# Optimization experiments

Measured on AMD Instinct MI355X. Metric: run time of the kernel, lower is better.

## Reference

```python
import jax, jax.numpy as jnp
import numpy as np

M = 10000      # spans with antecedents
KMAX = 30      # max antecedents per span
N = 12000      # total candidate spans (rows of g_i)
GDIM = 512     # span embedding dim
DDIM, GEDIM, SDIM = 20, 20, 20  # distance / genre / speaker embed dims
HID = 150      # Score hidden dim
GIJ = 3 * GDIM + DDIM + GEDIM + SDIM  # 1596
NDIST, NGENRE, NSPK = 10, 7, 3


def setup_inputs() -> dict:
    rng = np.random.default_rng(0)
    lengths = rng.integers(1, KMAX + 1, size=M)           # antecedents per span
    P = int(lengths.sum())
    seg_ids = np.repeat(np.arange(1, M + 1), lengths).astype(np.int32)  # segment 0 is the leading empty split
    pos_in_seg = np.concatenate([np.arange(l) for l in lengths]).astype(np.int32)
    seg_lengths = np.concatenate([[0], lengths]).astype(np.int32)        # [S], S = M+1
    mention_ids = rng.integers(0, N, size=P).astype(np.int32)
    antecedent_ids = rng.integers(0, N, size=P).astype(np.int32)
    dist_idx = rng.integers(0, NDIST, size=P).astype(np.int32)
    genre_idx = rng.integers(0, NGENRE, size=P).astype(np.int32)
    speaker_idx = rng.integers(0, NSPK, size=P).astype(np.int32)

    ks = jax.random.split(jax.random.key(0), 12)
    sc = lambda d: 1.0 / np.sqrt(d)
    return {
        'g_i': jax.random.normal(ks[0], (N, GDIM), jnp.float32),
        'mention_scores': jax.random.normal(ks[1], (N, 1), jnp.float32),
        'dist_emb': jax.random.normal(ks[2], (NDIST, DDIM), jnp.float32),
        'genre_emb': jax.random.normal(ks[3], (NGENRE, GEDIM), jnp.float32),
        'speaker_emb': jax.random.normal(ks[4], (NSPK, SDIM), jnp.float32),
        'W1': jax.random.normal(ks[5], (GIJ, HID), jnp.float32) * sc(GIJ),
        'b1': jnp.zeros((HID,), jnp.float32),
        'W2': jax.random.normal(ks[6], (HID, HID), jnp.float32) * sc(HID),
        'b2': jnp.zeros((HID,), jnp.float32),
        'W3': jax.random.normal(ks[7], (HID, 1), jnp.float32) * sc(HID),
        'b3': jnp.zeros((1,), jnp.float32),
        'mention_ids': jnp.asarray(mention_ids),
        'antecedent_ids': jnp.asarray(antecedent_ids),
        'dist_idx': jnp.asarray(dist_idx),
        'genre_idx': jnp.asarray(genre_idx),
        'speaker_idx': jnp.asarray(speaker_idx),
        'seg_ids': jnp.asarray(seg_ids),
        'pos_in_seg': jnp.asarray(pos_in_seg),
        'seg_lengths': jnp.asarray(seg_lengths),
    }


def reference(g_i, mention_scores, dist_emb, genre_emb, speaker_emb,
              W1, b1, W2, b2, W3, b3,
              mention_ids, antecedent_ids, dist_idx, genre_idx, speaker_idx,
              seg_ids, pos_in_seg, seg_lengths):
    # phi = cat(distance, genre, speaker) side features, [P, 60]
    phi = jnp.concatenate([dist_emb[dist_idx], genre_emb[genre_idx], speaker_emb[speaker_idx]], axis=1)
    i_g = g_i[mention_ids]      # [P, GDIM] irregular gather
    j_g = g_i[antecedent_ids]   # [P, GDIM]
    pairs = jnp.concatenate([i_g, j_g, i_g * j_g, phi], axis=1)  # [P, GIJ]
    # 3-layer MLP scorer (dropout is identity at inference)
    h = jax.nn.relu(pairs @ W1 + b1)
    h = jax.nn.relu(h @ W2 + b2)
    s_ij = (h @ W3 + b3)[:, 0]  # [P]
    coref = mention_scores[mention_ids, 0] + mention_scores[antecedent_ids, 0] + s_ij  # [P]
    # variable-length segment softmax with epsilon=0 appended, padded with 1000
    S = seg_lengths.shape[0]
    dense = jnp.full((S, KMAX + 1), -jnp.inf, jnp.float32)
    dense = dense.at[seg_ids, pos_in_seg].set(coref)
    dense = dense.at[jnp.arange(S), seg_lengths].set(0.0)  # epsilon slot
    probs = jax.nn.softmax(dense, axis=1)  # -inf slots -> 0
    col = jnp.arange(KMAX + 1)
    probs = jnp.where(col[None, :] > seg_lengths[:, None], 1000.0, probs)  # pad value 1000
    return probs  # [S, KMAX+1]
```

## Files before the change

### kernel.cpp

```cpp
#include <hip/hip_runtime.h>
#include <stdint.h>

#define GDIM   512
#define HID    150
#define HIDP   160
#define NROWS  12000
#define KP1    31
#define BMP    128
#define BMF    256

typedef __attribute__((ext_vector_type(4))) float f32x4;
typedef __attribute__((ext_vector_type(2))) float f32x2;
typedef long i64;

__device__ __forceinline__ unsigned short f2bf(float x){
    unsigned int u = __float_as_uint(x);
    return (unsigned short)((u + 0x7fffu + ((u >> 16) & 1u)) >> 16);
}
__device__ __forceinline__ float bf2f(unsigned short u){
    return __uint_as_float(((unsigned int)u) << 16);
}
__device__ __forceinline__ i64 u2l(uint2 v){ return __builtin_bit_cast(i64, v); }
__device__ __forceinline__ f32x4 mfma8(i64 a, i64 b, f32x4 c){
    return __builtin_amdgcn_mfma_f32_16x16x32_fp8_fp8(a, b, c, 0, 0, 0);
}
__device__ __forceinline__ uint2 f8mulpk(uint2 m, uint2 a){
    f32x2 m0 = __builtin_amdgcn_cvt_pk_f32_fp8(m.x, false);
    f32x2 m1 = __builtin_amdgcn_cvt_pk_f32_fp8(m.x, true);
    f32x2 m2 = __builtin_amdgcn_cvt_pk_f32_fp8(m.y, false);
    f32x2 m3 = __builtin_amdgcn_cvt_pk_f32_fp8(m.y, true);
    f32x2 a0 = __builtin_amdgcn_cvt_pk_f32_fp8(a.x, false);
    f32x2 a1 = __builtin_amdgcn_cvt_pk_f32_fp8(a.x, true);
    f32x2 a2 = __builtin_amdgcn_cvt_pk_f32_fp8(a.y, false);
    f32x2 a3 = __builtin_amdgcn_cvt_pk_f32_fp8(a.y, true);
    unsigned int r0 = 0, r1 = 0;
    r0 = __builtin_amdgcn_cvt_pk_fp8_f32(m0[0]*a0[0], m0[1]*a0[1], r0, false);
    r0 = __builtin_amdgcn_cvt_pk_fp8_f32(m1[0]*a1[0], m1[1]*a1[1], r0, true);
    r1 = __builtin_amdgcn_cvt_pk_fp8_f32(m2[0]*a2[0], m2[1]*a2[1], r1, false);
    r1 = __builtin_amdgcn_cvt_pk_fp8_f32(m3[0]*a3[0], m3[1]*a3[1], r1, true);
    return (uint2){r0, r1};
}
__device__ __forceinline__ void glds16(const void* g, void* l){
    __builtin_amdgcn_global_load_lds(
        (const __attribute__((address_space(1))) unsigned int*)g,
        (__attribute__((address_space(3))) unsigned int*)l, 16, 0, 0);
}

__global__ void k_prep0(const float* __restrict__ g, unsigned char* __restrict__ g8,
                        int* __restrict__ hist, int4* __restrict__ recs,
                        const float* __restrict__ W1, unsigned char* __restrict__ W18,
                        const float* __restrict__ W2, unsigned char* __restrict__ W28, int P){
    int i = blockIdx.x * blockDim.x + threadIdx.x;
    if (i < NROWS) hist[i] = 0;
    if (i < BMF) recs[P + i] = (int4){0, 0, (int)0x80000000, 0};
    if (i < 30720){
        int s = i / 10240, r = i % 10240;
        int n = r >> 6, gi = r & 63;
        int gdst = gi ^ (n & 7);
        int k0 = s * 512 + gi * 8;
        float x[8];
        #pragma unroll
        for (int e = 0; e < 8; e++) x[e] = (n < HID) ? W1[(size_t)(k0 + e) * HID + n] : 0.f;
        unsigned int d0 = 0, d1 = 0;
        d0 = __builtin_amdgcn_cvt_pk_fp8_f32(x[0], x[1], d0, false);
        d0 = __builtin_amdgcn_cvt_pk_fp8_f32(x[2], x[3], d0, true);
        d1 = __builtin_amdgcn_cvt_pk_fp8_f32(x[4], x[5], d1, false);
        d1 = __builtin_amdgcn_cvt_pk_fp8_f32(x[6], x[7], d1, true);
        *reinterpret_cast<uint2*>(W18 + (size_t)s * 81920 + n * 512 + gdst * 8) = (uint2){d0, d1};
    }
    if (i < 6912){
        int n2 = i / 42, kd = (i % 42) * 4;
        float y[4];
        #pragma unroll
        for (int e = 0; e < 4; e++){
            int k = kd + e;
            y[e] = (n2 < HID && k < HID) ? W2[(size_t)k * HID + n2] : 0.f;
        }
        unsigned int d = 0;
        d = __builtin_amdgcn_cvt_pk_fp8_f32(y[0], y[1], d, false);
        d = __builtin_amdgcn_cvt_pk_fp8_f32(y[2], y[3], d, true);
        reinterpret_cast<unsigned int*>(W28)[i] = d;
    }
    if (i >= NROWS * 32) return;
    int lh = i & 3, kt = (i >> 2) & 7, row = i >> 5;
    const float* src = g + (size_t)row * 512 + kt * 64 + lh * 8;
    float4 x0 = *reinterpret_cast<const float4*>(src);
    float4 x1 = *reinterpret_cast<const float4*>(src + 4);
    float4 x2 = *reinterpret_cast<const float4*>(src + 32);
    float4 x3 = *reinterpret_cast<const float4*>(src + 36);
    uint4 o; unsigned int d;
    d = 0; d = __builtin_amdgcn_cvt_pk_fp8_f32(x0.x, x0.y, d, false);
    d = __builtin_amdgcn_cvt_pk_fp8_f32(x0.z, x0.w, d, true);  o.x = d;
    d = 0; d = __builtin_amdgcn_cvt_pk_fp8_f32(x1.x, x1.y, d, false);
    d = __builtin_amdgcn_cvt_pk_fp8_f32(x1.z, x1.w, d, true);  o.y = d;
    d = 0; d = __builtin_amdgcn_cvt_pk_fp8_f32(x2.x, x2.y, d, false);
    d = __builtin_amdgcn_cvt_pk_fp8_f32(x2.z, x2.w, d, true);  o.z = d;
    d = 0; d = __builtin_amdgcn_cvt_pk_fp8_f32(x3.x, x3.y, d, false);
    d = __builtin_amdgcn_cvt_pk_fp8_f32(x3.z, x3.w, d, true);  o.w = d;
    *reinterpret_cast<uint4*>(g8 + (size_t)row * 512 + kt * 64 + lh * 16) = o;
}

__global__ void k_wprep(const float* __restrict__ de, const float* __restrict__ ge,
                        const float* __restrict__ se, const float* __restrict__ W1,
                        const float* __restrict__ b1,
                        const float* __restrict__ W3, const float* __restrict__ b2,
                        unsigned short* __restrict__ PhiW,
                        float* __restrict__ w3p, float* __restrict__ b2p){
    int c = blockIdx.x, tid = threadIdx.x;
    if (c < 210 && tid < HIDP){
        int si = c % 3, gi2 = (c / 3) % 7, di = c / 21;
        float acc = 0.f;
        if (tid < HID){
            acc = b1[tid];
            #pragma unroll
            for (int dd = 0; dd < 20; dd++) acc += de[di*20 + dd] * W1[(size_t)(1536 + dd) * HID + tid];
            #pragma unroll
            for (int dd = 0; dd < 20; dd++) acc += ge[gi2*20 + dd] * W1[(size_t)(1556 + dd) * HID + tid];
            #pragma unroll
            for (int dd = 0; dd < 20; dd++) acc += se[si*20 + dd] * W1[(size_t)(1576 + dd) * HID + tid];
        }
        PhiW[c * HIDP + tid] = f2bf(acc);
    }
    if (c == 210 && tid < HIDP){
        w3p[tid] = (tid < HID) ? W3[tid] : 0.f;
        b2p[tid] = (tid < HID) ? b2[tid] : 0.f;
    }
}

__global__ void k_hist(const int* __restrict__ mid, int* __restrict__ hist, int P){
    int p = blockIdx.x * blockDim.x + threadIdx.x;
    if (p < P) atomicAdd(&hist[mid[p]], 1);
}
__global__ void k_scan(const int* __restrict__ hist, int* __restrict__ offsw, int nb){
    __shared__ int part[1024];
    int t = threadIdx.x;
    int chunk = (nb + 1023) / 1024;
    int lo = t * chunk, hi = lo + chunk; if (hi > nb) hi = nb;
    int s = 0;
    for (int b = lo; b < hi; b++) s += hist[b];
    part[t] = s;
    __syncthreads();
    for (int d = 1; d < 1024; d <<= 1){
        int v = (t >= d) ? part[t - d] : 0;
        __syncthreads();
        part[t] += v;
        __syncthreads();
    }
    int run = part[t] - s;
    for (int b = lo; b < hi; b++){ offsw[b] = run; run += hist[b]; }
}
__global__ void k_scatter(const int* __restrict__ mident, const int* __restrict__ antid,
                          const int* __restrict__ di, const int* __restrict__ gi, const int* __restrict__ si,
                          const int* __restrict__ seg, const int* __restrict__ pos, const float* __restrict__ ms,
                          int* __restrict__ offsw, int4* __restrict__ recs, int P){
    int p = blockIdx.x * blockDim.x + threadIdx.x;
    if (p >= P) return;
    int m = mident[p], a = antid[p];
    int idx = atomicAdd(&offsw[m], 1);
    int combo = (di[p] * 7 + gi[p]) * 3 + si[p];
    int meta = (combo << 19) | (seg[p] << 5) | pos[p];
    int4 r; r.x = m; r.y = a; r.z = meta; r.w = __float_as_int(ms[m] + ms[a]);
    recs[idx] = r;
}

__global__ __launch_bounds__(256) void k_proj(const unsigned char* __restrict__ g8,
                                              const unsigned char* __restrict__ W18,
                                              unsigned char* __restrict__ out){
    __shared__ __align__(16) char smem[81920];
    const unsigned char* Wt = W18 + (size_t)blockIdx.y * 81920;
    unsigned char* outh = out + (size_t)blockIdx.y * NROWS * HIDP;
    int tid = threadIdx.x, lane = tid & 63, w = tid >> 6;
    int l15 = lane & 15, lh = lane >> 4;
    int swz8 = (l15 & 7) << 3;
    int row0 = blockIdx.x * BMP;

    int r0 = row0 + 32*w + l15;       int r0c = (r0 < NROWS) ? r0 : NROWS - 1;
    int r1 = r0 + 16;                 int r1c = (r1 < NROWS) ? r1 : NROWS - 1;
    const unsigned char* gp0 = g8 + (size_t)r0c * GDIM + lh * 16;
    const unsigned char* gp1 = g8 + (size_t)r1c * GDIM + lh * 16;

    #pragma unroll
    for (int i = 0; i < 20; i++){
        int c = w * 20 + i;
        glds16(Wt + c * 1024 + lane * 16, smem + c * 1024);
    }

    f32x4 acc1[10][2];
    #pragma unroll
    for (int t = 0; t < 10; t++){ acc1[t][0] = (f32x4){0,0,0,0}; acc1[t][1] = (f32x4){0,0,0,0}; }

    asm volatile("s_waitcnt vmcnt(0)" ::: "memory");
    __builtin_amdgcn_s_barrier();

    uint4 R0 = *reinterpret_cast<const uint4*>(gp0);
    uint4 R1 = *reinterpret_cast<const uint4*>(gp1);
    #pragma unroll
    for (int kt = 0; kt < 8; kt++){
        uint4 N0, N1;
        if (kt < 7){
            N0 = *reinterpret_cast<const uint4*>(gp0 + (kt+1)*64);
            N1 = *reinterpret_cast<const uint4*>(gp1 + (kt+1)*64);
        }
        i64 a00 = u2l((uint2){R0.x, R0.y}), a01 = u2l((uint2){R0.z, R0.w});
        i64 a10 = u2l((uint2){R1.x, R1.y}), a11 = u2l((uint2){R1.z, R1.w});
        #pragma unroll
        for (int t = 0; t < 10; t++){
            int rowb = (t*16 + l15) * 512;
            i64 b0 = *reinterpret_cast<const i64*>(&smem[rowb + ((kt*64 +  0 + lh*8) ^ swz8)]);
            i64 b1 = *reinterpret_cast<const i64*>(&smem[rowb + ((kt*64 + 32 + lh*8) ^ swz8)]);
            acc1[t][0] = mfma8(b0, a00, acc1[t][0]);
            acc1[t][1] = mfma8(b0, a10, acc1[t][1]);
            acc1[t][0] = mfma8(b1, a01, acc1[t][0]);
            acc1[t][1] = mfma8(b1, a11, acc1[t][1]);
        }
        R0 = N0; R1 = N1;
    }

    #pragma unroll
    for (int rf = 0; rf < 2; rf++){
        int row = row0 + 32*w + 16*rf + l15;
        if (row < NROWS){
            #pragma unroll
            for (int t = 0; t < 10; t++){
                f32x4 a = acc1[t][rf];
                unsigned int dw = 0;
                dw = __builtin_amdgcn_cvt_pk_fp8_f32(a[0], a[1], dw, false);
                dw = __builtin_amdgcn_cvt_pk_fp8_f32(a[2], a[3], dw, true);
                *reinterpret_cast<unsigned int*>(outh + (size_t)row * HIDP + 16*t + 4*lh) = dw;
            }
        }
    }
}

__global__ __launch_bounds__(512, 2) void k_fused(
    const unsigned char* __restrict__ g8,
    const unsigned char* __restrict__ W1c8, const unsigned char* __restrict__ W28,
    const unsigned short* __restrict__ PhiW, const unsigned char* __restrict__ Am,
    const unsigned char* __restrict__ Aa,
    const float* __restrict__ w3p, const float* __restrict__ b2p, const float* __restrict__ b3,
    const int4* __restrict__ recs,
    float* __restrict__ dense)
{
    __shared__ __align__(16) char smem[81920];
    int tid = threadIdx.x, lane = tid & 63, w = tid >> 6;
    int l15 = lane & 15, lh = lane >> 4;
    int swz8 = (l15 & 7) << 3;

    int nwg = gridDim.x, orig = blockIdx.x, bid = orig;
    if (nwg >= 8){
        int q = nwg >> 3, r = nwg & 7;
        int xcd = orig & 7, lid = orig >> 3;
        bid = (xcd < r ? xcd * (q + 1) : r * (q + 1) + (xcd - r) * q) + lid;
    }
    int p0 = bid * BMF;

    int4 rec0 = recs[p0 + 32*w + l15];
    int4 rec1 = recs[p0 + 32*w + 16 + l15];

    const unsigned char* gm0 = g8 + (size_t)rec0.x * GDIM + lh * 16;
    const unsigned char* ga0 = g8 + (size_t)rec0.y * GDIM + lh * 16;
    const unsigned char* gm1 = g8 + (size_t)rec1.x * GDIM + lh * 16;
    const unsigned char* ga1 = g8 + (size_t)rec1.y * GDIM + lh * 16;

    #pragma unroll
    for (int i = 0; i < 10; i++){
        int c = w * 10 + i;
        glds16(W1c8 + c * 1024 + lane * 16, smem + c * 1024);
    }

    f32x4 acc1[10][2];
    #pragma unroll
    for (int t = 0; t < 10; t++){ acc1[t][0] = (f32x4){0,0,0,0}; acc1[t][1] = (f32x4){0,0,0,0}; }

    asm volatile("s_waitcnt vmcnt(0)" ::: "memory");
    __builtin_amdgcn_s_barrier();

    uint4 Rm0 = *reinterpret_cast<const uint4*>(gm0);
    uint4 Ra0 = *reinterpret_cast<const uint4*>(ga0);
    uint4 Rm1 = *reinterpret_cast<const uint4*>(gm1);
    uint4 Ra1 = *reinterpret_cast<const uint4*>(ga1);
    #pragma unroll
    for (int kt = 0; kt < 8; kt++){
        uint4 Nm0, Na0, Nm1, Na1;
        if (kt < 7){
            Nm0 = *reinterpret_cast<const uint4*>(gm0 + (kt+1)*64);
            Na0 = *reinterpret_cast<const uint4*>(ga0 + (kt+1)*64);
            Nm1 = *reinterpret_cast<const uint4*>(gm1 + (kt+1)*64);
            Na1 = *reinterpret_cast<const uint4*>(ga1 + (kt+1)*64);
        }
        uint2 p00 = f8mulpk((uint2){Rm0.x, Rm0.y}, (uint2){Ra0.x, Ra0.y});
        uint2 p01 = f8mulpk((uint2){Rm0.z, Rm0.w}, (uint2){Ra0.z, Ra0.w});
        uint2 p10 = f8mulpk((uint2){Rm1.x, Rm1.y}, (uint2){Ra1.x, Ra1.y});
        uint2 p11 = f8mulpk((uint2){Rm1.z, Rm1.w}, (uint2){Ra1.z, Ra1.w});
        i64 lp00 = u2l(p00), lp01 = u2l(p01), lp10 = u2l(p10), lp11 = u2l(p11);
        #pragma unroll
        for (int t = 0; t < 10; t++){
            int rowb = (t*16 + l15) * 512;
            i64 b0 = *reinterpret_cast<const i64*>(&smem[rowb + ((kt*64 +  0 + lh*8) ^ swz8)]);
            i64 b1 = *reinterpret_cast<const i64*>(&smem[rowb + ((kt*64 + 32 + lh*8) ^ swz8)]);
            acc1[t][0] = mfma8(b0, lp00, acc1[t][0]);
            acc1[t][1] = mfma8(b0, lp10, acc1[t][1]);
            acc1[t][0] = mfma8(b1, lp01, acc1[t][0]);
            acc1[t][1] = mfma8(b1, lp11, acc1[t][1]);
        }
        Rm0 = Nm0; Ra0 = Na0; Rm1 = Nm1; Ra1 = Na1;
    }

    asm volatile("s_waitcnt lgkmcnt(0)" ::: "memory");
    __builtin_amdgcn_s_barrier();

    #pragma unroll
    for (int i = 0; i < 4; i++){
        int c = w * 4 + i;
        if (c < 27) glds16(W28 + c * 1024 + lane * 16, smem + 43008 + c * 1024);
    }

    #pragma unroll
    for (int rf = 0; rf < 2; rf++){
        int4 rc = rf ? rec1 : rec0;
        int pr = 32*w + 16*rf + l15;
        const unsigned char* amp = Am + (size_t)rc.x * HIDP;
        const unsigned char* aap = Aa + (size_t)rc.y * HIDP;
        int combo = (rc.z >> 19) & 0xFF;
        const unsigned short* php = PhiW + (size_t)combo * HIDP;
        char* h1row = smem + pr * 168;
        #pragma unroll
        for (int t = 0; t < 10; t++){
            int h0 = 16*t + 4*lh;
            unsigned int amd = *reinterpret_cast<const unsigned int*>(amp + h0);
            unsigned int aad = *reinterpret_cast<const unsigned int*>(aap + h0);
            ushort4 ph4 = *reinterpret_cast<const ushort4*>(php + h0);
            f32x2 amL = __builtin_amdgcn_cvt_pk_f32_fp8(amd, false);
            f32x2 amH = __builtin_amdgcn_cvt_pk_f32_fp8(amd, true);
            f32x2 aaL = __builtin_amdgcn_cvt_pk_f32_fp8(aad, false);
            f32x2 aaH = __builtin_amdgcn_cvt_pk_f32_fp8(aad, true);
            f32x4 a = acc1[t][rf];
            float v0 = fmaxf(a[0] + amL[0] + aaL[0] + bf2f(ph4.x), 0.f);
            float v1 = fmaxf(a[1] + amL[1] + aaL[1] + bf2f(ph4.y), 0.f);
            float v2 = fmaxf(a[2] + amH[0] + aaH[0] + bf2f(ph4.z), 0.f);
            float v3 = fmaxf(a[3] + amH[1] + aaH[1] + bf2f(ph4.w), 0.f);
            unsigned int dw = 0;
            dw = __builtin_amdgcn_cvt_pk_fp8_f32(v0, v1, dw, false);
            dw = __builtin_amdgcn_cvt_pk_fp8_f32(v2, v3, dw, true);
            *reinterpret_cast<unsigned int*>(h1row + h0) = dw;
        }
    }

    asm volatile("s_waitcnt vmcnt(0) lgkmcnt(0)" ::: "memory");
    __builtin_amdgcn_s_barrier();

    f32x4 acc2[10][2];
    #pragma unroll
    for (int t = 0; t < 10; t++){ acc2[t][0] = (f32x4){0,0,0,0}; acc2[t][1] = (f32x4){0,0,0,0}; }
    const char* w2b = smem + 43008;
    #pragma unroll
    for (int k2 = 0; k2 < 5; k2++){
        i64 h0f = *reinterpret_cast<const i64*>(smem + (32*w + l15)      * 168 + k2*32 + lh*8);
        i64 h1f = *reinterpret_cast<const i64*>(smem + (32*w + 16 + l15) * 168 + k2*32 + lh*8);
        #pragma unroll
        for (int t = 0; t < 10; t++){
            i64 wf = *reinterpret_cast<const i64*>(w2b + (16*t + l15) * 168 + k2*32 + lh*8);
            acc2[t][0] = mfma8(wf, h0f, acc2[t][0]);
            acc2[t][1] = mfma8(wf, h1f, acc2[t][1]);
        }
    }

    float b3v = b3[0];
    #pragma unroll
    for (int rf = 0; rf < 2; rf++){
        int4 rc = rf ? rec1 : rec0;
        float s = 0.f;
        #pragma unroll
        for (int t = 0; t < 10; t++){
            f32x4 w3v = *reinterpret_cast<const f32x4*>(w3p + 16*t + 4*lh);
            f32x4 b2v = *reinterpret_cast<const f32x4*>(b2p + 16*t + 4*lh);
            f32x4 a = acc2[t][rf];
            s += fmaxf(a[0] + b2v[0], 0.f) * w3v[0];
            s += fmaxf(a[1] + b2v[1], 0.f) * w3v[1];
            s += fmaxf(a[2] + b2v[2], 0.f) * w3v[2];
            s += fmaxf(a[3] + b2v[3], 0.f) * w3v[3];
        }
        s += __shfl_xor(s, 16);
        s += __shfl_xor(s, 32);
        if (!(rc.z & 0x80000000) && lh == 0){
            float val = s + b3v + __int_as_float(rc.w);
            dense[(size_t)((rc.z >> 5) & 0x3FFF) * KP1 + (rc.z & 31)] = val;
        }
    }
}

__global__ void k_softmax(const float* __restrict__ dense, const int* __restrict__ seg_lengths,
                          float* __restrict__ out, int S){
    int wid = threadIdx.x >> 6, lane = threadIdx.x & 63;
    int s = blockIdx.x * 4 + wid;
    if (s >= S) return;
    int len = seg_lengths[s];
    float ninf = -__builtin_inff();
    float val = ninf;
    if (lane < KP1) val = (lane < len) ? dense[(size_t)s * KP1 + lane] : ((lane == len) ? 0.f : ninf);
    float m = val;
    #pragma unroll
    for (int msk = 1; msk < 64; msk <<= 1) m = fmaxf(m, __shfl_xor(m, msk));
    float e = expf(val - m);
    float sum = e;
    #pragma unroll
    for (int msk = 1; msk < 64; msk <<= 1) sum += __shfl_xor(sum, msk);
    if (lane < KP1) out[(size_t)s * KP1 + lane] = (lane > len) ? 1000.f : (e / sum);
}

extern "C" void kernel_launch(void* const* d_in, const int* in_sizes, int n_in,
                              void* d_out, int out_size, void* d_ws, size_t ws_size,
                              hipStream_t stream){
    const float* g_i        = (const float*)d_in[0];
    const float* ms         = (const float*)d_in[1];
    const float* dist_emb   = (const float*)d_in[2];
    const float* genre_emb  = (const float*)d_in[3];
    const float* spk_emb    = (const float*)d_in[4];
    const float* W1         = (const float*)d_in[5];
    const float* b1         = (const float*)d_in[6];
    const float* W2         = (const float*)d_in[7];
    const float* b2         = (const float*)d_in[8];
    const float* W3         = (const float*)d_in[9];
    const float* b3         = (const float*)d_in[10];
    const int* mention_ids  = (const int*)d_in[11];
    const int* antecedent_ids = (const int*)d_in[12];
    const int* dist_idx     = (const int*)d_in[13];
    const int* genre_idx    = (const int*)d_in[14];
    const int* spk_idx      = (const int*)d_in[15];
    const int* seg_ids      = (const int*)d_in[16];
    const int* pos_in_seg   = (const int*)d_in[17];
    const int* seg_lengths  = (const int*)d_in[18];
    int P = in_sizes[11];
    int S = in_sizes[18];

    char* ws = (char*)d_ws;
    unsigned char* W18   = (unsigned char*)(ws + 0);
    unsigned char* W28   = (unsigned char*)(ws + 245760);
    unsigned short* PhiW = (unsigned short*)(ws + 273408);
    float* w3pad         = (float*)(ws + 340608);
    float* b2pad         = (float*)(ws + 341248);
    unsigned char* g8    = (unsigned char*)(ws + 341888);
    unsigned char* Am8   = (unsigned char*)(ws + 6485888);
    unsigned char* Aa8   = (unsigned char*)(ws + 8405888);
    int* hist            = (int*)(ws + 10325888);
    int* offsw           = (int*)(ws + 10373888);
    int4* recs           = (int4*)(ws + 10421888);
    float* dense         = (float*)(ws + 13000192);

    k_prep0<<<1500, 256, 0, stream>>>(g_i, g8, hist, recs, W1, W18, W2, W28, P);
    k_wprep<<<211, 256, 0, stream>>>(dist_emb, genre_emb, spk_emb, W1, b1, W3, b2,
                                     PhiW, w3pad, b2pad);
    k_hist<<<(P + 255)/256, 256, 0, stream>>>(mention_ids, hist, P);
    k_scan<<<1, 1024, 0, stream>>>(hist, offsw, NROWS);
    k_scatter<<<(P + 255)/256, 256, 0, stream>>>(mention_ids, antecedent_ids, dist_idx, genre_idx,
        spk_idx, seg_ids, pos_in_seg, ms, offsw, recs, P);

    k_proj<<<dim3((NROWS + BMP - 1)/BMP, 2), 256, 0, stream>>>(g8, W18, Am8);

    k_fused<<<(P + BMF - 1)/BMF, 512, 0, stream>>>(g8, W18 + 2*81920, W28, PhiW,
        Am8, Aa8, w3pad, b2pad, b3, recs, dense);

    k_softmax<<<(S + 3)/4, 256, 0, stream>>>(dense, seg_lengths, (float*)d_out, S);
}
```

Baseline: 129.5 us.

## Halve fused tile and LDS, stream W1 in two K-halves, merge prep kernels

```diff
diff --git a/kernel.cpp b/kernel.cpp
--- a/kernel.cpp
+++ b/kernel.cpp
@@ -7,7 +7,7 @@
 #define NROWS  12000
 #define KP1    31
 #define BMP    128
-#define BMF    256
+#define BMF    128
 
 typedef __attribute__((ext_vector_type(4))) float f32x4;
 typedef __attribute__((ext_vector_type(2))) float f32x2;
@@ -49,14 +49,20 @@
 __global__ void k_prep0(const float* __restrict__ g, unsigned char* __restrict__ g8,
                         int* __restrict__ hist, int4* __restrict__ recs,
                         const float* __restrict__ W1, unsigned char* __restrict__ W18,
-                        const float* __restrict__ W2, unsigned char* __restrict__ W28, int P){
+                        const float* __restrict__ W2, unsigned char* __restrict__ W28,
+                        const float* __restrict__ de, const float* __restrict__ ge,
+                        const float* __restrict__ se, const float* __restrict__ b1,
+                        const float* __restrict__ W3, const float* __restrict__ b2,
+                        unsigned short* __restrict__ PhiW,
+                        float* __restrict__ w3p, float* __restrict__ b2p, int P){
     int i = blockIdx.x * blockDim.x + threadIdx.x;
     if (i < NROWS) hist[i] = 0;
     if (i < BMF) recs[P + i] = (int4){0, 0, (int)0x80000000, 0};
     if (i < 30720){
         int s = i / 10240, r = i % 10240;
         int n = r >> 6, gi = r & 63;
-        int gdst = gi ^ (n & 7);
+        int hf = gi >> 5, gih = gi & 31;
+        int gdst = gih ^ (n & 7);
         int k0 = s * 512 + gi * 8;
         float x[8];
         #pragma unroll
@@ -66,7 +72,7 @@
         d0 = __builtin_amdgcn_cvt_pk_fp8_f32(x[2], x[3], d0, true);
         d1 = __builtin_amdgcn_cvt_pk_fp8_f32(x[4], x[5], d1, false);
         d1 = __builtin_amdgcn_cvt_pk_fp8_f32(x[6], x[7], d1, true);
-        *reinterpret_cast<uint2*>(W18 + (size_t)s * 81920 + n * 512 + gdst * 8) = (uint2){d0, d1};
+        *reinterpret_cast<uint2*>(W18 + (size_t)s * 81920 + hf * 40960 + n * 256 + gdst * 8) = (uint2){d0, d1};
     }
     if (i < 6912){
         int n2 = i / 42, kd = (i % 42) * 4;
@@ -81,49 +87,42 @@
         d = __builtin_amdgcn_cvt_pk_fp8_f32(y[2], y[3], d, true);
         reinterpret_cast<unsigned int*>(W28)[i] = d;
     }
-    if (i >= NROWS * 32) return;
-    int lh = i & 3, kt = (i >> 2) & 7, row = i >> 5;
-    const float* src = g + (size_t)row * 512 + kt * 64 + lh * 8;
-    float4 x0 = *reinterpret_cast<const float4*>(src);
-    float4 x1 = *reinterpret_cast<const float4*>(src + 4);
-    float4 x2 = *reinterpret_cast<const float4*>(src + 32);
-    float4 x3 = *reinterpret_cast<const float4*>(src + 36);
-    uint4 o; unsigned int d;
-    d = 0; d = __builtin_amdgcn_cvt_pk_fp8_f32(x0.x, x0.y, d, false);
-    d = __builtin_amdgcn_cvt_pk_fp8_f32(x0.z, x0.w, d, true);  o.x = d;
-    d = 0; d = __builtin_amdgcn_cvt_pk_fp8_f32(x1.x, x1.y, d, false);
-    d = __builtin_amdgcn_cvt_pk_fp8_f32(x1.z, x1.w, d, true);  o.y = d;
-    d = 0; d = __builtin_amdgcn_cvt_pk_fp8_f32(x2.x, x2.y, d, false);
-    d = __builtin_amdgcn_cvt_pk_fp8_f32(x2.z, x2.w, d, true);  o.z = d;
-    d = 0; d = __builtin_amdgcn_cvt_pk_fp8_f32(x3.x, x3.y, d, false);
-    d = __builtin_amdgcn_cvt_pk_fp8_f32(x3.z, x3.w, d, true);  o.w = d;
-    *reinterpret_cast<uint4*>(g8 + (size_t)row * 512 + kt * 64 + lh * 16) = o;
-}
-
-__global__ void k_wprep(const float* __restrict__ de, const float* __restrict__ ge,
-                        const float* __restrict__ se, const float* __restrict__ W1,
-                        const float* __restrict__ b1,
-                        const float* __restrict__ W3, const float* __restrict__ b2,
-                        unsigned short* __restrict__ PhiW,
-                        float* __restrict__ w3p, float* __restrict__ b2p){
-    int c = blockIdx.x, tid = threadIdx.x;
-    if (c < 210 && tid < HIDP){
+    if (i < NROWS * 32){
+        int lh = i & 3, kt = (i >> 2) & 7, row = i >> 5;
+        const float* src = g + (size_t)row * 512 + kt * 64 + lh * 8;
+        float4 x0 = *reinterpret_cast<const float4*>(src);
+        float4 x1 = *reinterpret_cast<const float4*>(src + 4);
+        float4 x2 = *reinterpret_cast<const float4*>(src + 32);
+        float4 x3 = *reinterpret_cast<const float4*>(src + 36);
+        uint4 o; unsigned int d;
+        d = 0; d = __builtin_amdgcn_cvt_pk_fp8_f32(x0.x, x0.y, d, false);
+        d = __builtin_amdgcn_cvt_pk_fp8_f32(x0.z, x0.w, d, true);  o.x = d;
+        d = 0; d = __builtin_amdgcn_cvt_pk_fp8_f32(x1.x, x1.y, d, false);
+        d = __builtin_amdgcn_cvt_pk_fp8_f32(x1.z, x1.w, d, true);  o.y = d;
+        d = 0; d = __builtin_amdgcn_cvt_pk_fp8_f32(x2.x, x2.y, d, false);
+        d = __builtin_amdgcn_cvt_pk_fp8_f32(x2.z, x2.w, d, true);  o.z = d;
+        d = 0; d = __builtin_amdgcn_cvt_pk_fp8_f32(x3.x, x3.y, d, false);
+        d = __builtin_amdgcn_cvt_pk_fp8_f32(x3.z, x3.w, d, true);  o.w = d;
+        *reinterpret_cast<uint4*>(g8 + (size_t)row * 512 + kt * 64 + lh * 16) = o;
+    } else if (i < NROWS * 32 + 33600){
+        int j = i - NROWS * 32;
+        int c = j / HIDP, h = j - c * HIDP;
         int si = c % 3, gi2 = (c / 3) % 7, di = c / 21;
         float acc = 0.f;
-        if (tid < HID){
-            acc = b1[tid];
-            #pragma unroll
-            for (int dd = 0; dd < 20; dd++) acc += de[di*20 + dd] * W1[(size_t)(1536 + dd) * HID + tid];
-            #pragma unroll
-            for (int dd = 0; dd < 20; dd++) acc += ge[gi2*20 + dd] * W1[(size_t)(1556 + dd) * HID + tid];
-            #pragma unroll
-            for (int dd = 0; dd < 20; dd++) acc += se[si*20 + dd] * W1[(size_t)(1576 + dd) * HID + tid];
-        }
-        PhiW[c * HIDP + tid] = f2bf(acc);
-    }
-    if (c == 210 && tid < HIDP){
-        w3p[tid] = (tid < HID) ? W3[tid] : 0.f;
-        b2p[tid] = (tid < HID) ? b2[tid] : 0.f;
+        if (h < HID){
+            acc = b1[h];
+            #pragma unroll
+            for (int dd = 0; dd < 20; dd++) acc += de[di*20 + dd] * W1[(size_t)(1536 + dd) * HID + h];
+            #pragma unroll
+            for (int dd = 0; dd < 20; dd++) acc += ge[gi2*20 + dd] * W1[(size_t)(1556 + dd) * HID + h];
+            #pragma unroll
+            for (int dd = 0; dd < 20; dd++) acc += se[si*20 + dd] * W1[(size_t)(1576 + dd) * HID + h];
+        }
+        PhiW[c * HIDP + h] = f2bf(acc);
+    } else if (i < NROWS * 32 + 33600 + HIDP){
+        int h = i - NROWS * 32 - 33600;
+        w3p[h] = (h < HID) ? W3[h] : 0.f;
+        b2p[h] = (h < HID) ? b2[h] : 0.f;
     }
 }
 
@@ -166,7 +165,7 @@
 __global__ __launch_bounds__(256) void k_proj(const unsigned char* __restrict__ g8,
                                               const unsigned char* __restrict__ W18,
                                               unsigned char* __restrict__ out){
-    __shared__ __align__(16) char smem[81920];
+    __shared__ __align__(16) char smem[40960];
     const unsigned char* Wt = W18 + (size_t)blockIdx.y * 81920;
     unsigned char* outh = out + (size_t)blockIdx.y * NROWS * HIDP;
     int tid = threadIdx.x, lane = tid & 63, w = tid >> 6;
@@ -179,41 +178,47 @@
     const unsigned char* gp0 = g8 + (size_t)r0c * GDIM + lh * 16;
     const unsigned char* gp1 = g8 + (size_t)r1c * GDIM + lh * 16;
 
-    #pragma unroll
-    for (int i = 0; i < 20; i++){
-        int c = w * 20 + i;
-        glds16(Wt + c * 1024 + lane * 16, smem + c * 1024);
-    }
-
     f32x4 acc1[10][2];
     #pragma unroll
     for (int t = 0; t < 10; t++){ acc1[t][0] = (f32x4){0,0,0,0}; acc1[t][1] = (f32x4){0,0,0,0}; }
 
-    asm volatile("s_waitcnt vmcnt(0)" ::: "memory");
-    __builtin_amdgcn_s_barrier();
-
-    uint4 R0 = *reinterpret_cast<const uint4*>(gp0);
-    uint4 R1 = *reinterpret_cast<const uint4*>(gp1);
-    #pragma unroll
-    for (int kt = 0; kt < 8; kt++){
-        uint4 N0, N1;
-        if (kt < 7){
-            N0 = *reinterpret_cast<const uint4*>(gp0 + (kt+1)*64);
-            N1 = *reinterpret_cast<const uint4*>(gp1 + (kt+1)*64);
-        }
-        i64 a00 = u2l((uint2){R0.x, R0.y}), a01 = u2l((uint2){R0.z, R0.w});
-        i64 a10 = u2l((uint2){R1.x, R1.y}), a11 = u2l((uint2){R1.z, R1.w});
-        #pragma unroll
-        for (int t = 0; t < 10; t++){
-            int rowb = (t*16 + l15) * 512;
-            i64 b0 = *reinterpret_cast<const i64*>(&smem[rowb + ((kt*64 +  0 + lh*8) ^ swz8)]);
-            i64 b1 = *reinterpret_cast<const i64*>(&smem[rowb + ((kt*64 + 32 + lh*8) ^ swz8)]);
-            acc1[t][0] = mfma8(b0, a00, acc1[t][0]);
-            acc1[t][1] = mfma8(b0, a10, acc1[t][1]);
-            acc1[t][0] = mfma8(b1, a01, acc1[t][0]);
-            acc1[t][1] = mfma8(b1, a11, acc1[t][1]);
-        }
-        R0 = N0; R1 = N1;
+    #pragma unroll
+    for (int hf = 0; hf < 2; hf++){
+        #pragma unroll
+        for (int i = 0; i < 10; i++){
+            int c = w * 10 + i;
+            glds16(Wt + hf * 40960 + c * 1024 + lane * 16, smem + c * 1024);
+        }
+        asm volatile("s_waitcnt vmcnt(0)" ::: "memory");
+        __builtin_amdgcn_s_barrier();
+
+        const unsigned char* a0p = gp0 + hf * 256;
+        const unsigned char* a1p = gp1 + hf * 256;
+        uint4 R0 = *reinterpret_cast<const uint4*>(a0p);
+        uint4 R1 = *reinterpret_cast<const uint4*>(a1p);
+        #pragma unroll
+        for (int kt = 0; kt < 4; kt++){
+            uint4 N0, N1;
+            if (kt < 3){
+                N0 = *reinterpret_cast<const uint4*>(a0p + (kt+1)*64);
+                N1 = *reinterpret_cast<const uint4*>(a1p + (kt+1)*64);
+            }
+            i64 a00 = u2l((uint2){R0.x, R0.y}), a01 = u2l((uint2){R0.z, R0.w});
+            i64 a10 = u2l((uint2){R1.x, R1.y}), a11 = u2l((uint2){R1.z, R1.w});
+            #pragma unroll
+            for (int t = 0; t < 10; t++){
+                int rowb = (t*16 + l15) * 256;
+                i64 b0 = *reinterpret_cast<const i64*>(&smem[rowb + ((kt*64 +  0 + lh*8) ^ swz8)]);
+                i64 b1 = *reinterpret_cast<const i64*>(&smem[rowb + ((kt*64 + 32 + lh*8) ^ swz8)]);
+                acc1[t][0] = mfma8(b0, a00, acc1[t][0]);
+                acc1[t][1] = mfma8(b0, a10, acc1[t][1]);
+                acc1[t][0] = mfma8(b1, a01, acc1[t][0]);
+                acc1[t][1] = mfma8(b1, a11, acc1[t][1]);
+            }
+            R0 = N0; R1 = N1;
+        }
+        asm volatile("s_waitcnt lgkmcnt(0)" ::: "memory");
+        __builtin_amdgcn_s_barrier();
     }
 
     #pragma unroll
@@ -232,7 +237,7 @@
     }
 }
 
-__global__ __launch_bounds__(512, 2) void k_fused(
+__global__ __launch_bounds__(256) void k_fused(
     const unsigned char* __restrict__ g8,
     const unsigned char* __restrict__ W1c8, const unsigned char* __restrict__ W28,
     const unsigned short* __restrict__ PhiW, const unsigned char* __restrict__ Am,
@@ -241,7 +246,7 @@
     const int4* __restrict__ recs,
     float* __restrict__ dense)
 {
-    __shared__ __align__(16) char smem[81920];
+    __shared__ __align__(16) char smem[40960];
     int tid = threadIdx.x, lane = tid & 63, w = tid >> 6;
     int l15 = lane & 15, lh = lane >> 4;
     int swz8 = (l15 & 7) << 3;
@@ -262,57 +267,56 @@
     const unsigned char* gm1 = g8 + (size_t)rec1.x * GDIM + lh * 16;
     const unsigned char* ga1 = g8 + (size_t)rec1.y * GDIM + lh * 16;
 
-    #pragma unroll
-    for (int i = 0; i < 10; i++){
-        int c = w * 10 + i;
-        glds16(W1c8 + c * 1024 + lane * 16, smem + c * 1024);
-    }
-
     f32x4 acc1[10][2];
     #pragma unroll
     for (int t = 0; t < 10; t++){ acc1[t][0] = (f32x4){0,0,0,0}; acc1[t][1] = (f32x4){0,0,0,0}; }
 
-    asm volatile("s_waitcnt vmcnt(0)" ::: "memory");
-    __builtin_amdgcn_s_barrier();
-
-    uint4 Rm0 = *reinterpret_cast<const uint4*>(gm0);
-    uint4 Ra0 = *reinterpret_cast<const uint4*>(ga0);
-    uint4 Rm1 = *reinterpret_cast<const uint4*>(gm1);
-    uint4 Ra1 = *reinterpret_cast<const uint4*>(ga1);
-    #pragma unroll
-    for (int kt = 0; kt < 8; kt++){
-        uint4 Nm0, Na0, Nm1, Na1;
-        if (kt < 7){
-            Nm0 = *reinterpret_cast<const uint4*>(gm0 + (kt+1)*64);
-            Na0 = *reinterpret_cast<const uint4*>(ga0 + (kt+1)*64);
-            Nm1 = *reinterpret_cast<const uint4*>(gm1 + (kt+1)*64);
-            Na1 = *reinterpret_cast<const uint4*>(ga1 + (kt+1)*64);
-        }
-        uint2 p00 = f8mulpk((uint2){Rm0.x, Rm0.y}, (uint2){Ra0.x, Ra0.y});
-        uint2 p01 = f8mulpk((uint2){Rm0.z, Rm0.w}, (uint2){Ra0.z, Ra0.w});
-        uint2 p10 = f8mulpk((uint2){Rm1.x, Rm1.y}, (uint2){Ra1.x, Ra1.y});
-        uint2 p11 = f8mulpk((uint2){Rm1.z, Rm1.w}, (uint2){Ra1.z, Ra1.w});
-        i64 lp00 = u2l(p00), lp01 = u2l(p01), lp10 = u2l(p10), lp11 = u2l(p11);
-        #pragma unroll
-        for (int t = 0; t < 10; t++){
-            int rowb = (t*16 + l15) * 512;
-            i64 b0 = *reinterpret_cast<const i64*>(&smem[rowb + ((kt*64 +  0 + lh*8) ^ swz8)]);
-            i64 b1 = *reinterpret_cast<const i64*>(&smem[rowb + ((kt*64 + 32 + lh*8) ^ swz8)]);
-            acc1[t][0] = mfma8(b0, lp00, acc1[t][0]);
-            acc1[t][1] = mfma8(b0, lp10, acc1[t][1]);
-            acc1[t][0] = mfma8(b1, lp01, acc1[t][0]);
-            acc1[t][1] = mfma8(b1, lp11, acc1[t][1]);
-        }
-        Rm0 = Nm0; Ra0 = Na0; Rm1 = Nm1; Ra1 = Na1;
-    }
-
-    asm volatile("s_waitcnt lgkmcnt(0)" ::: "memory");
-    __builtin_amdgcn_s_barrier();
-
-    #pragma unroll
-    for (int i = 0; i < 4; i++){
-        int c = w * 4 + i;
-        if (c < 27) glds16(W28 + c * 1024 + lane * 16, smem + 43008 + c * 1024);
+    #pragma unroll
+    for (int hf = 0; hf < 2; hf++){
+        #pragma unroll
+        for (int i = 0; i < 10; i++){
+            int c = w * 10 + i;
+            glds16(W1c8 + hf * 40960 + c * 1024 + lane * 16, smem + c * 1024);
+        }
+        asm volatile("s_waitcnt vmcnt(0)" ::: "memory");
+        __builtin_amdgcn_s_barrier();
+
+        const unsigned char* m0p = gm0 + hf * 256;
+        const unsigned char* a0p = ga0 + hf * 256;
+        const unsigned char* m1p = gm1 + hf * 256;
+        const unsigned char* a1p = ga1 + hf * 256;
+        uint4 Rm0 = *reinterpret_cast<const uint4*>(m0p);
+        uint4 Ra0 = *reinterpret_cast<const uint4*>(a0p);
+        uint4 Rm1 = *reinterpret_cast<const uint4*>(m1p);
+        uint4 Ra1 = *reinterpret_cast<const uint4*>(a1p);
+        #pragma unroll
+        for (int kt = 0; kt < 4; kt++){
+            uint4 Nm0, Na0, Nm1, Na1;
+            if (kt < 3){
+                Nm0 = *reinterpret_cast<const uint4*>(m0p + (kt+1)*64);
+                Na0 = *reinterpret_cast<const uint4*>(a0p + (kt+1)*64);
+                Nm1 = *reinterpret_cast<const uint4*>(m1p + (kt+1)*64);
+                Na1 = *reinterpret_cast<const uint4*>(a1p + (kt+1)*64);
+            }
+            uint2 p00 = f8mulpk((uint2){Rm0.x, Rm0.y}, (uint2){Ra0.x, Ra0.y});
+            uint2 p01 = f8mulpk((uint2){Rm0.z, Rm0.w}, (uint2){Ra0.z, Ra0.w});
+            uint2 p10 = f8mulpk((uint2){Rm1.x, Rm1.y}, (uint2){Ra1.x, Ra1.y});
+            uint2 p11 = f8mulpk((uint2){Rm1.z, Rm1.w}, (uint2){Ra1.z, Ra1.w});
+            i64 lp00 = u2l(p00), lp01 = u2l(p01), lp10 = u2l(p10), lp11 = u2l(p11);
+            #pragma unroll
+            for (int t = 0; t < 10; t++){
+                int rowb = (t*16 + l15) * 256;
+                i64 b0 = *reinterpret_cast<const i64*>(&smem[rowb + ((kt*64 +  0 + lh*8) ^ swz8)]);
+                i64 b1 = *reinterpret_cast<const i64*>(&smem[rowb + ((kt*64 + 32 + lh*8) ^ swz8)]);
+                acc1[t][0] = mfma8(b0, lp00, acc1[t][0]);
+                acc1[t][1] = mfma8(b0, lp10, acc1[t][1]);
+                acc1[t][0] = mfma8(b1, lp01, acc1[t][0]);
+                acc1[t][1] = mfma8(b1, lp11, acc1[t][1]);
+            }
+            Rm0 = Nm0; Ra0 = Na0; Rm1 = Nm1; Ra1 = Na1;
+        }
+        asm volatile("s_waitcnt lgkmcnt(0)" ::: "memory");
+        __builtin_amdgcn_s_barrier();
     }
 
     #pragma unroll
@@ -346,20 +350,16 @@
         }
     }
 
-    asm volatile("s_waitcnt vmcnt(0) lgkmcnt(0)" ::: "memory");
-    __builtin_amdgcn_s_barrier();
-
     f32x4 acc2[10][2];
     #pragma unroll
     for (int t = 0; t < 10; t++){ acc2[t][0] = (f32x4){0,0,0,0}; acc2[t][1] = (f32x4){0,0,0,0}; }
-    const char* w2b = smem + 43008;
     #pragma unroll
     for (int k2 = 0; k2 < 5; k2++){
         i64 h0f = *reinterpret_cast<const i64*>(smem + (32*w + l15)      * 168 + k2*32 + lh*8);
         i64 h1f = *reinterpret_cast<const i64*>(smem + (32*w + 16 + l15) * 168 + k2*32 + lh*8);
         #pragma unroll
         for (int t = 0; t < 10; t++){
-            i64 wf = *reinterpret_cast<const i64*>(w2b + (16*t + l15) * 168 + k2*32 + lh*8);
+            i64 wf = *reinterpret_cast<const i64*>(W28 + (16*t + l15) * 168 + k2*32 + lh*8);
             acc2[t][0] = mfma8(wf, h0f, acc2[t][0]);
             acc2[t][1] = mfma8(wf, h1f, acc2[t][1]);
         }
@@ -447,9 +447,9 @@
     int4* recs           = (int4*)(ws + 10421888);
     float* dense         = (float*)(ws + 13000192);
 
-    k_prep0<<<1500, 256, 0, stream>>>(g_i, g8, hist, recs, W1, W18, W2, W28, P);
-    k_wprep<<<211, 256, 0, stream>>>(dist_emb, genre_emb, spk_emb, W1, b1, W3, b2,
-                                     PhiW, w3pad, b2pad);
+    int prep_threads = NROWS * 32 + 33600 + HIDP;
+    k_prep0<<<(prep_threads + 255)/256, 256, 0, stream>>>(g_i, g8, hist, recs, W1, W18, W2, W28,
+        dist_emb, genre_emb, spk_emb, b1, W3, b2, PhiW, w3pad, b2pad, P);
     k_hist<<<(P + 255)/256, 256, 0, stream>>>(mention_ids, hist, P);
     k_scan<<<1, 1024, 0, stream>>>(hist, offsw, NROWS);
     k_scatter<<<(P + 255)/256, 256, 0, stream>>>(mention_ids, antecedent_ids, dist_idx, genre_idx,
@@ -457,7 +457,7 @@
 
     k_proj<<<dim3((NROWS + BMP - 1)/BMP, 2), 256, 0, stream>>>(g8, W18, Am8);
 
-    k_fused<<<(P + BMF - 1)/BMF, 512, 0, stream>>>(g8, W18 + 2*81920, W28, PhiW,
+    k_fused<<<(P + BMF - 1)/BMF, 256, 0, stream>>>(g8, W18 + 2*81920, W28, PhiW,
         Am8, Aa8, w3pad, b2pad, b3, recs, dense);
 
     k_softmax<<<(S + 3)/4, 256, 0, stream>>>(dense, seg_lengths, (float*)d_out, S);
```

New measurement: 142.7 us. +10.2%, slower.
